# Kernel tuning notes

Measured on AMD Instinct MI355X. Metric: run time of the kernel, lower is better.

## Reference

```python
import jax, jax.numpy as jnp
import numpy as np

N_NODES = 100000
N_FEAT = 128
N_CLASSES = 40
N_EDGES = 1600000
K_HOPS = 2


def setup_inputs() -> dict:
    key = jax.random.key(0)
    k1, k2, k3 = jax.random.split(key, 3)
    x = jax.random.normal(k1, (N_NODES, N_FEAT), dtype=jnp.float32)
    edge_index = jax.random.randint(k2, (2, N_EDGES), 0, N_NODES, dtype=jnp.int32)
    W = jax.random.normal(k3, (N_FEAT, N_CLASSES), dtype=jnp.float32) * 0.05
    b = jnp.zeros((N_CLASSES,), dtype=jnp.float32)
    return {"x": x, "W": W, "b": b, "edge_index": edge_index, "K": K_HOPS}


def reference(x, W, b, edge_index, K):
    N = x.shape[0]
    src, dst = edge_index[0], edge_index[1]
    # Add self-loops (GCN normalization, as in PyG gcn_norm)
    loop = jnp.arange(N, dtype=src.dtype)
    src = jnp.concatenate([src, loop])
    dst = jnp.concatenate([dst, loop])
    # Symmetric normalization: deg^{-1/2} A_hat deg^{-1/2}
    deg = jnp.zeros((N,), dtype=x.dtype).at[dst].add(jnp.ones_like(dst, dtype=x.dtype))
    deg_inv_sqrt = jnp.where(deg > 0, jax.lax.rsqrt(jnp.maximum(deg, 1.0)), 0.0)
    norm = deg_inv_sqrt[src] * deg_inv_sqrt[dst]  # [E+N]
    for _ in range(K):
        msgs = norm[:, None] * x[src]  # gather [E+N, F]
        x = jax.ops.segment_sum(msgs, dst, num_segments=N)
    logits = x @ W + b  # [N, C]
    return jax.nn.log_softmax(logits, axis=1)
```

## Files before the change

kernel.cpp:

```cpp
#include <hip/hip_runtime.h>
#include <math.h>


#define FDIM 128
#define CDIM 40
#define C4   10
#define BKT_SHIFT 8
#define NB   512
#define NBLK 512
#define NPB  51

__device__ __forceinline__ unsigned int bf16rn(float f) {
    unsigned int u = __float_as_uint(f);
    return (u + 0x7fffu + ((u >> 16) & 1u)) >> 16;
}
__device__ __forceinline__ unsigned int pack2(float lo, float hi) {
    unsigned int a = bf16rn(lo);
    unsigned int b = __float_as_uint(hi);
    b = (b + 0x7fffu + ((b >> 16) & 1u)) & 0xffff0000u;
    return a | b;
}
__device__ __forceinline__ void addu4(uint4 u, float* a) {
    a[0] += __uint_as_float(u.x << 16);
    a[1] += __uint_as_float(u.x & 0xffff0000u);
    a[2] += __uint_as_float(u.y << 16);
    a[3] += __uint_as_float(u.y & 0xffff0000u);
    a[4] += __uint_as_float(u.z << 16);
    a[5] += __uint_as_float(u.z & 0xffff0000u);
    a[6] += __uint_as_float(u.w << 16);
    a[7] += __uint_as_float(u.w & 0xffff0000u);
}

__global__ void hist_k(const int* __restrict__ dst, int* __restrict__ G,
                       int E, int EB) {
    __shared__ int h[NB];
    int t = threadIdx.x;
    for (int i = t; i < NB; i += 256) h[i] = 0;
    __syncthreads();
    int s = blockIdx.x * EB;
    int e = min(s + EB, E);
    for (int i = s + t; i < e; i += 256)
        atomicAdd(&h[dst[i] >> BKT_SHIFT], 1);
    __syncthreads();
    for (int i = t; i < NB; i += 256) G[blockIdx.x * NB + i] = h[i];
}

__global__ void colscan_k(int* __restrict__ G, int* __restrict__ T) {
    __shared__ int lds[256];
    int j = blockIdx.x;
    int t = threadIdx.x;
    int v0 = G[(2 * t) * NB + j];
    int v1 = G[(2 * t + 1) * NB + j];
    int s = v0 + v1;
    lds[t] = s;
    __syncthreads();
    for (int off = 1; off < 256; off <<= 1) {
        int a = (t >= off) ? lds[t - off] : 0;
        __syncthreads();
        lds[t] += a;
        __syncthreads();
    }
    int excl = lds[t] - s;
    G[(2 * t) * NB + j] = excl;
    G[(2 * t + 1) * NB + j] = excl + v0;
    if (t == 255) T[j] = lds[255];
}

__global__ void bscan_k(const int* __restrict__ T, int* __restrict__ bs) {
    __shared__ int lds[256];
    int t = threadIdx.x;
    int v0 = T[2 * t];
    int v1 = T[2 * t + 1];
    int s = v0 + v1;
    lds[t] = s;
    __syncthreads();
    for (int off = 1; off < 256; off <<= 1) {
        int a = (t >= off) ? lds[t - off] : 0;
        __syncthreads();
        lds[t] += a;
        __syncthreads();
    }
    int excl = lds[t] - s;
    bs[2 * t] = excl;
    bs[2 * t + 1] = excl + v0;
    if (t == 255) bs[NB] = lds[255];
}

__global__ void part_k(const int* __restrict__ src, const int* __restrict__ dst,
                       const int* __restrict__ G, const int* __restrict__ bs,
                       unsigned int* __restrict__ tmp, int E, int EB) {
    __shared__ int offs[NB];
    __shared__ int cur[NB];
    int t = threadIdx.x;
    for (int i = t; i < NB; i += 256) {
        offs[i] = bs[i] + G[blockIdx.x * NB + i];
        cur[i] = 0;
    }
    __syncthreads();
    int s = blockIdx.x * EB;
    int e = min(s + EB, E);
    for (int i = s + t; i < e; i += 256) {
        int d = dst[i];
        int j = d >> BKT_SHIFT;
        int r = atomicAdd(&cur[j], 1);
        tmp[offs[j] + r] = (unsigned int)src[i] | ((unsigned int)(d & 255) << 24);
    }
}

__global__ void csr_k(const unsigned int* __restrict__ tmp, const int* __restrict__ bs,
                      int* __restrict__ rowptr, float* __restrict__ dinv,
                      float* __restrict__ dsq, int* __restrict__ col, int N, int E) {
    __shared__ int cnt[256];
    __shared__ int ptr[256];
    int j = blockIdx.x;
    int t = threadIdx.x;
    int base = j << BKT_SHIFT;
    int s = bs[j];
    int e = bs[j + 1];
    cnt[t] = 0;
    __syncthreads();
    for (int i = s + t; i < e; i += 256)
        atomicAdd(&cnt[tmp[i] >> 24], 1);
    __syncthreads();
    int v = cnt[t];
    ptr[t] = v;
    __syncthreads();
    for (int off = 1; off < 256; off <<= 1) {
        int a = (t >= off) ? ptr[t - off] : 0;
        __syncthreads();
        ptr[t] += a;
        __syncthreads();
    }
    int excl = ptr[t] - v;
    int node = base + t;
    if (node < N) {
        rowptr[node] = s + excl;
        float d = (float)(v + 1);
        dinv[node] = rsqrtf(d);
        dsq[node] = sqrtf(d);
    }
    if (j == 0 && t == 0) rowptr[N] = E;
    cnt[t] = excl;
    __syncthreads();
    for (int i = s + t; i < e; i += 256) {
        unsigned int p = tmp[i];
        int loc = p >> 24;
        int r = atomicAdd(&cnt[loc], 1);
        col[s + r] = (int)(p & 0xFFFFFF);
    }
}

__global__ __launch_bounds__(256) void gemm_k(const float* __restrict__ x,
                                              const float* __restrict__ W,
                                              const float* __restrict__ dinv,
                                              uint4* __restrict__ Zbf, int n) {
    int node = blockIdx.x * 256 + threadIdx.x;
    if (node >= n) return;
    float acc[CDIM];
    #pragma unroll
    for (int c = 0; c < CDIM; ++c) acc[c] = 0.f;
    const float4* xr = (const float4*)(x + (size_t)node * FDIM);
    for (int ch = 0; ch < 8; ++ch) {
        float4 xv0 = xr[ch * 4 + 0];
        float4 xv1 = xr[ch * 4 + 1];
        float4 xv2 = xr[ch * 4 + 2];
        float4 xv3 = xr[ch * 4 + 3];
        const float* wb = W + ch * 16 * CDIM;
        const float xs[16] = {xv0.x, xv0.y, xv0.z, xv0.w,
                              xv1.x, xv1.y, xv1.z, xv1.w,
                              xv2.x, xv2.y, xv2.z, xv2.w,
                              xv3.x, xv3.y, xv3.z, xv3.w};
        #pragma unroll
        for (int f = 0; f < 16; ++f) {
            float s = xs[f];
            const float* wr = wb + f * CDIM;
            #pragma unroll
            for (int c = 0; c < CDIM; ++c)
                acc[c] += s * wr[c];
        }
    }
    float di = dinv[node];
    uint4* zp = Zbf + (size_t)node * 5;
    #pragma unroll
    for (int g = 0; g < 5; ++g) {
        uint4 o;
        o.x = pack2(acc[g * 8 + 0] * di, acc[g * 8 + 1] * di);
        o.y = pack2(acc[g * 8 + 2] * di, acc[g * 8 + 3] * di);
        o.z = pack2(acc[g * 8 + 4] * di, acc[g * 8 + 5] * di);
        o.w = pack2(acc[g * 8 + 6] * di, acc[g * 8 + 7] * di);
        zp[g] = o;
    }
}

template <bool FINAL>
__global__ __launch_bounds__(256) void prop_k(const int* __restrict__ rowptr,
                                              const int* __restrict__ col,
                                              const float* __restrict__ dinv,
                                              const float* __restrict__ dsq,
                                              const float* __restrict__ bias,
                                              const uint4* __restrict__ Zin,
                                              uint4* __restrict__ Zout_bf,
                                              float* __restrict__ out_f32, int n) {
    __shared__ float bsm[CDIM];
    __shared__ float red[256];
    int t = threadIdx.x;
    if (FINAL && t < CDIM) bsm[t] = bias[t];
    int g = t / 5;
    int c8 = t - g * 5;
    int node = blockIdx.x * NPB + g;
    bool active = (g < NPB) && (node < n);
    float acc[8];
    #pragma unroll
    for (int c = 0; c < 8; ++c) acc[c] = 0.f;
    float w = 0.f;
    if (active) {
        float di = dinv[node];
        w = di * di;
        addu4(Zin[(size_t)node * 5 + c8], acc);
        int e = rowptr[node];
        int end = rowptr[node + 1];
        for (; e + 3 < end; e += 4) {
            int s0 = col[e], s1 = col[e + 1], s2 = col[e + 2], s3 = col[e + 3];
            uint4 a0 = Zin[(size_t)s0 * 5 + c8];
            uint4 a1 = Zin[(size_t)s1 * 5 + c8];
            uint4 a2 = Zin[(size_t)s2 * 5 + c8];
            uint4 a3 = Zin[(size_t)s3 * 5 + c8];
            addu4(a0, acc); addu4(a1, acc); addu4(a2, acc); addu4(a3, acc);
        }
        for (; e < end; ++e)
            addu4(Zin[(size_t)col[e] * 5 + c8], acc);
    }

    if (!FINAL) {
        if (active) {
            uint4 o;
            o.x = pack2(acc[0] * w, acc[1] * w);
            o.y = pack2(acc[2] * w, acc[3] * w);
            o.z = pack2(acc[4] * w, acc[5] * w);
            o.w = pack2(acc[6] * w, acc[7] * w);
            Zout_bf[(size_t)node * 5 + c8] = o;
        }
        return;
    }

    __syncthreads();
    float v[8];
    float m8 = -INFINITY;
    if (active) {
        float ws_ = w * dsq[node];
        #pragma unroll
        for (int j = 0; j < 8; ++j) {
            v[j] = acc[j] * ws_ + bsm[c8 * 8 + j];
            m8 = fmaxf(m8, v[j]);
        }
    }
    red[t] = m8;
    __syncthreads();
    float m = m8;
    if (active) {
        int rb = g * 5;
        m = fmaxf(fmaxf(fmaxf(red[rb], red[rb + 1]), fmaxf(red[rb + 2], red[rb + 3])),
                  red[rb + 4]);
    }
    float s8 = 0.f;
    if (active) {
        #pragma unroll
        for (int j = 0; j < 8; ++j) s8 += expf(v[j] - m);
    }
    __syncthreads();
    red[t] = s8;
    __syncthreads();
    if (active) {
        int rb = g * 5;
        float s = (red[rb] + red[rb + 1]) + (red[rb + 2] + red[rb + 3]) + red[rb + 4];
        float ls = m + logf(s);
        float* p = out_f32 + (size_t)node * CDIM + c8 * 8;
        *(float4*)p = make_float4(v[0] - ls, v[1] - ls, v[2] - ls, v[3] - ls);
        *(float4*)(p + 4) = make_float4(v[4] - ls, v[5] - ls, v[6] - ls, v[7] - ls);
    }
}

extern "C" void kernel_launch(void* const* d_in, const int* in_sizes, int n_in,
                              void* d_out, int out_size, void* d_ws, size_t ws_size,
                              hipStream_t stream) {
    const float* x = (const float*)d_in[0];
    const float* W = (const float*)d_in[1];
    const float* b = (const float*)d_in[2];
    const int* ei = (const int*)d_in[3];

    int C = in_sizes[2];
    int F = in_sizes[1] / C;
    int N = in_sizes[0] / F;
    int E = in_sizes[3] / 2;
    const int* src = ei;
    const int* dst = ei + E;

    char* ws = (char*)d_ws;
    size_t goff = 0;
    int* G = (int*)(ws + goff);                       goff += (size_t)NBLK * NB * 4;
    int* T = (int*)(ws + goff);                       goff += (size_t)NB * 4;
    int* bs = (int*)(ws + goff);                      goff += (size_t)(NB + 1) * 4 + 12;
    goff = (goff + 15) & ~(size_t)15;
    unsigned int* tmp = (unsigned int*)(ws + goff);   goff += (size_t)E * 4;
    size_t z0bytes = (size_t)N * 80;
    size_t unionEnd = (z0bytes > goff) ? z0bytes : goff;
    unionEnd = (unionEnd + 15) & ~(size_t)15;
    uint4* Z0bf = (uint4*)ws;
    size_t off = unionEnd;
    int* rowptr = (int*)(ws + off); off += ((size_t)(N + 1) * 4 + 15) & ~(size_t)15;
    float* dinv = (float*)(ws + off); off += ((size_t)N * 4 + 15) & ~(size_t)15;
    float* dsq = (float*)(ws + off); off += ((size_t)N * 4 + 15) & ~(size_t)15;
    int* col = (int*)(ws + off); off += ((size_t)E * 4 + 15) & ~(size_t)15;
    uint4* Zb = (uint4*)(ws + off); off += (z0bytes + 15) & ~(size_t)15;

    int EB = (E + NBLK - 1) / NBLK;
    int NBr = (N + 255) >> BKT_SHIFT;

    hist_k<<<NBLK, 256, 0, stream>>>(dst, G, E, EB);
    colscan_k<<<NB, 256, 0, stream>>>(G, T);
    bscan_k<<<1, 256, 0, stream>>>(T, bs);
    part_k<<<NBLK, 256, 0, stream>>>(src, dst, G, bs, tmp, E, EB);
    csr_k<<<NBr, 256, 0, stream>>>(tmp, bs, rowptr, dinv, dsq, col, N, E);

    gemm_k<<<(N + 255) / 256, 256, 0, stream>>>(x, W, dinv, Z0bf, N);

    int pgrid = (N + NPB - 1) / NPB;
    prop_k<false><<<pgrid, 256, 0, stream>>>(rowptr, col, dinv, dsq, b,
                                             Z0bf, Zb, nullptr, N);
    prop_k<true><<<pgrid, 256, 0, stream>>>(rowptr, col, dinv, dsq, b,
                                            Zb, nullptr, (float*)d_out, N);
}
```

Measured before the change: 248.4 us.

## Restructure dense projection to stage node tile in LDS and split classes across wavefronts

The projection kernel no longer has each thread compute all 40 outputs for one node from a privately loaded row. It now stages a 64-node tile of x transposed into shared memory, and five wavefronts each compute an 8-class slice with wave-uniform W loads. The aim is to cut per-thread register pressure (40 accumulators plus unrolled weights) and raise occupancy. The cost is a shared-memory transpose with strided writes, which may cause bank conflicts, plus a block-wide barrier.

```diff
diff --git a/kernel.cpp b/kernel.cpp
--- a/kernel.cpp
+++ b/kernel.cpp
@@ -150,45 +150,50 @@
     }
 }
 
-__global__ __launch_bounds__(256) void gemm_k(const float* __restrict__ x,
+__global__ __launch_bounds__(320) void gemm_k(const float* __restrict__ x,
                                               const float* __restrict__ W,
                                               const float* __restrict__ dinv,
                                               uint4* __restrict__ Zbf, int n) {
-    int node = blockIdx.x * 256 + threadIdx.x;
-    if (node >= n) return;
-    float acc[CDIM];
+    __shared__ float xT[FDIM][64];
+    int t = threadIdx.x;
+    int base = blockIdx.x * 64;
+    for (int i = t; i < 2048; i += 320) {
+        int nl = i & 63;
+        int f4 = i >> 6;
+        int node = base + nl;
+        float4 xv = make_float4(0.f, 0.f, 0.f, 0.f);
+        if (node < n) xv = *(const float4*)(x + (size_t)node * FDIM + f4 * 4);
+        xT[f4 * 4 + 0][nl] = xv.x;
+        xT[f4 * 4 + 1][nl] = xv.y;
+        xT[f4 * 4 + 2][nl] = xv.z;
+        xT[f4 * 4 + 3][nl] = xv.w;
+    }
+    int cg = __builtin_amdgcn_readfirstlane(t >> 6);
+    int ng = t & 63;
+    float acc[8];
     #pragma unroll
-    for (int c = 0; c < CDIM; ++c) acc[c] = 0.f;
-    const float4* xr = (const float4*)(x + (size_t)node * FDIM);
-    for (int ch = 0; ch < 8; ++ch) {
-        float4 xv0 = xr[ch * 4 + 0];
-        float4 xv1 = xr[ch * 4 + 1];
-        float4 xv2 = xr[ch * 4 + 2];
-        float4 xv3 = xr[ch * 4 + 3];
-        const float* wb = W + ch * 16 * CDIM;
-        const float xs[16] = {xv0.x, xv0.y, xv0.z, xv0.w,
-                              xv1.x, xv1.y, xv1.z, xv1.w,
-                              xv2.x, xv2.y, xv2.z, xv2.w,
-                              xv3.x, xv3.y, xv3.z, xv3.w};
-        #pragma unroll
-        for (int f = 0; f < 16; ++f) {
-            float s = xs[f];
-            const float* wr = wb + f * CDIM;
-            #pragma unroll
-            for (int c = 0; c < CDIM; ++c)
-                acc[c] += s * wr[c];
-        }
-    }
-    float di = dinv[node];
-    uint4* zp = Zbf + (size_t)node * 5;
-    #pragma unroll
-    for (int g = 0; g < 5; ++g) {
+    for (int c = 0; c < 8; ++c) acc[c] = 0.f;
+    __syncthreads();
+    const float* wbase = W + cg * 8;
+    #pragma unroll 4
+    for (int f = 0; f < FDIM; ++f) {
+        float xv = xT[f][ng];
+        float4 w0 = *(const float4*)(wbase + f * CDIM);
+        float4 w1 = *(const float4*)(wbase + f * CDIM + 4);
+        acc[0] += xv * w0.x; acc[1] += xv * w0.y;
+        acc[2] += xv * w0.z; acc[3] += xv * w0.w;
+        acc[4] += xv * w1.x; acc[5] += xv * w1.y;
+        acc[6] += xv * w1.z; acc[7] += xv * w1.w;
+    }
+    int node = base + ng;
+    if (node < n) {
+        float di = dinv[node];
         uint4 o;
-        o.x = pack2(acc[g * 8 + 0] * di, acc[g * 8 + 1] * di);
-        o.y = pack2(acc[g * 8 + 2] * di, acc[g * 8 + 3] * di);
-        o.z = pack2(acc[g * 8 + 4] * di, acc[g * 8 + 5] * di);
-        o.w = pack2(acc[g * 8 + 6] * di, acc[g * 8 + 7] * di);
-        zp[g] = o;
+        o.x = pack2(acc[0] * di, acc[1] * di);
+        o.y = pack2(acc[2] * di, acc[3] * di);
+        o.z = pack2(acc[4] * di, acc[5] * di);
+        o.w = pack2(acc[6] * di, acc[7] * di);
+        Zbf[(size_t)node * 5 + cg] = o;
     }
 }
 
@@ -322,7 +327,7 @@
     part_k<<<NBLK, 256, 0, stream>>>(src, dst, G, bs, tmp, E, EB);
     csr_k<<<NBr, 256, 0, stream>>>(tmp, bs, rowptr, dinv, dsq, col, N, E);
 
-    gemm_k<<<(N + 255) / 256, 256, 0, stream>>>(x, W, dinv, Z0bf, N);
+    gemm_k<<<(N + 63) / 64, 320, 0, stream>>>(x, W, dinv, Z0bf, N);
 
     int pgrid = (N + NPB - 1) / NPB;
     prop_k<false><<<pgrid, 256, 0, stream>>>(rowptr, col, dinv, dsq, b,
```

Result: faster. 233.6 us (-6.0%).

## Compute feature projection with split-bf16 MFMA instead of scalar FP32 FMAs

Applied to the files above, without the earlier changes.

Replaces the per-thread scalar FP32 GEMM (x @ W) with a wave-level MFMA 16x16x32 bf16 kernel. Both operands are split into bf16 hi and lo parts, and three products are summed to keep near-FP32 accuracy. A one-block prep kernel pre-swizzles W into the MFMA fragment layout. The epilogue stages results through shared memory so they can be scaled by dinv and packed to bf16. This targets the compute-bound scalar GEMM at the cost of an extra launch and some precision loss from the dropped lo*lo term.

```diff
diff --git a/kernel.cpp b/kernel.cpp
--- a/kernel.cpp
+++ b/kernel.cpp
@@ -9,6 +9,9 @@
 #define NB   512
 #define NBLK 512
 #define NPB  51
+
+typedef __attribute__((ext_vector_type(4))) float floatx4;
+typedef __attribute__((ext_vector_type(8))) short bshort8;
 
 __device__ __forceinline__ unsigned int bf16rn(float f) {
     unsigned int u = __float_as_uint(f);
@@ -150,45 +153,124 @@
     }
 }
 
+__global__ __launch_bounds__(256) void wprep_k(const float* __restrict__ W,
+                                               uint4* __restrict__ WF) {
+    int t = threadIdx.x;
+    for (int s = t; s < 768; s += 256) {
+        int l = s & 63;
+        int g = s >> 6;
+        int nt = g >> 2;
+        int ch = g & 3;
+        int c = nt * 16 + (l & 15);
+        int kb = ch * 32 + ((l >> 4) << 3);
+        unsigned int hw[4], lw[4];
+        #pragma unroll
+        for (int jw = 0; jw < 4; ++jw) {
+            unsigned int hs[2], ls[2];
+            #pragma unroll
+            for (int e = 0; e < 2; ++e) {
+                int j = jw * 2 + e;
+                float w = (c < CDIM) ? W[(kb + j) * CDIM + c] : 0.f;
+                unsigned int u = __float_as_uint(w);
+                float wh = __uint_as_float(u & 0xffff0000u);
+                float wr = w - wh;
+                hs[e] = u >> 16;
+                ls[e] = __float_as_uint(wr) >> 16;
+            }
+            hw[jw] = hs[0] | (hs[1] << 16);
+            lw[jw] = ls[0] | (ls[1] << 16);
+        }
+        WF[g * 64 + l] = make_uint4(hw[0], hw[1], hw[2], hw[3]);
+        WF[768 + g * 64 + l] = make_uint4(lw[0], lw[1], lw[2], lw[3]);
+    }
+}
+
+__device__ __forceinline__ void split8(const float* p, bshort8& hi, bshort8& lo) {
+    float4 a = *(const float4*)p;
+    float4 b = *(const float4*)(p + 4);
+    float f[8] = {a.x, a.y, a.z, a.w, b.x, b.y, b.z, b.w};
+    #pragma unroll
+    for (int j = 0; j < 8; ++j) {
+        unsigned int u = __float_as_uint(f[j]);
+        float r = f[j] - __uint_as_float(u & 0xffff0000u);
+        hi[j] = (short)(u >> 16);
+        lo[j] = (short)(__float_as_uint(r) >> 16);
+    }
+}
+
+#define EPS 52
+
 __global__ __launch_bounds__(256) void gemm_k(const float* __restrict__ x,
-                                              const float* __restrict__ W,
+                                              const uint4* __restrict__ WF,
                                               const float* __restrict__ dinv,
                                               uint4* __restrict__ Zbf, int n) {
-    int node = blockIdx.x * 256 + threadIdx.x;
-    if (node >= n) return;
-    float acc[CDIM];
+    __shared__ float ep[64 * EPS];
+    int t = threadIdx.x;
+    int wid = t >> 6;
+    int l = t & 63;
+    int lr = l & 15;
+    int lg = l >> 4;
+    int base64 = blockIdx.x * 64;
+    int mbase = base64 + wid * 16;
+    int node_a = mbase + lr;
+    bool arow_ok = node_a < n;
+    const bshort8* WFv = (const bshort8*)WF;
+
+    floatx4 acc0 = {0.f, 0.f, 0.f, 0.f};
+    floatx4 acc1 = {0.f, 0.f, 0.f, 0.f};
+    floatx4 acc2 = {0.f, 0.f, 0.f, 0.f};
+
     #pragma unroll
-    for (int c = 0; c < CDIM; ++c) acc[c] = 0.f;
-    const float4* xr = (const float4*)(x + (size_t)node * FDIM);
-    for (int ch = 0; ch < 8; ++ch) {
-        float4 xv0 = xr[ch * 4 + 0];
-        float4 xv1 = xr[ch * 4 + 1];
-        float4 xv2 = xr[ch * 4 + 2];
-        float4 xv3 = xr[ch * 4 + 3];
-        const float* wb = W + ch * 16 * CDIM;
-        const float xs[16] = {xv0.x, xv0.y, xv0.z, xv0.w,
-                              xv1.x, xv1.y, xv1.z, xv1.w,
-                              xv2.x, xv2.y, xv2.z, xv2.w,
-                              xv3.x, xv3.y, xv3.z, xv3.w};
-        #pragma unroll
-        for (int f = 0; f < 16; ++f) {
-            float s = xs[f];
-            const float* wr = wb + f * CDIM;
+    for (int ch = 0; ch < 4; ++ch) {
+        bshort8 ah, al;
+        if (arow_ok) {
+            split8(x + (size_t)node_a * FDIM + ch * 32 + lg * 8, ah, al);
+        } else {
             #pragma unroll
-            for (int c = 0; c < CDIM; ++c)
-                acc[c] += s * wr[c];
-        }
-    }
-    float di = dinv[node];
-    uint4* zp = Zbf + (size_t)node * 5;
+            for (int j = 0; j < 8; ++j) { ah[j] = 0; al[j] = 0; }
+        }
+        bshort8 bh0 = WFv[(0 * 4 + ch) * 64 + l];
+        bshort8 bl0 = WFv[768 + (0 * 4 + ch) * 64 + l];
+        bshort8 bh1 = WFv[(1 * 4 + ch) * 64 + l];
+        bshort8 bl1 = WFv[768 + (1 * 4 + ch) * 64 + l];
+        bshort8 bh2 = WFv[(2 * 4 + ch) * 64 + l];
+        bshort8 bl2 = WFv[768 + (2 * 4 + ch) * 64 + l];
+        acc0 = __builtin_amdgcn_mfma_f32_16x16x32_bf16(ah, bh0, acc0, 0, 0, 0);
+        acc0 = __builtin_amdgcn_mfma_f32_16x16x32_bf16(al, bh0, acc0, 0, 0, 0);
+        acc0 = __builtin_amdgcn_mfma_f32_16x16x32_bf16(ah, bl0, acc0, 0, 0, 0);
+        acc1 = __builtin_amdgcn_mfma_f32_16x16x32_bf16(ah, bh1, acc1, 0, 0, 0);
+        acc1 = __builtin_amdgcn_mfma_f32_16x16x32_bf16(al, bh1, acc1, 0, 0, 0);
+        acc1 = __builtin_amdgcn_mfma_f32_16x16x32_bf16(ah, bl1, acc1, 0, 0, 0);
+        acc2 = __builtin_amdgcn_mfma_f32_16x16x32_bf16(ah, bh2, acc2, 0, 0, 0);
+        acc2 = __builtin_amdgcn_mfma_f32_16x16x32_bf16(al, bh2, acc2, 0, 0, 0);
+        acc2 = __builtin_amdgcn_mfma_f32_16x16x32_bf16(ah, bl2, acc2, 0, 0, 0);
+    }
+
+    int nlb = wid * 16 + 4 * lg;
     #pragma unroll
-    for (int g = 0; g < 5; ++g) {
-        uint4 o;
-        o.x = pack2(acc[g * 8 + 0] * di, acc[g * 8 + 1] * di);
-        o.y = pack2(acc[g * 8 + 2] * di, acc[g * 8 + 3] * di);
-        o.z = pack2(acc[g * 8 + 4] * di, acc[g * 8 + 5] * di);
-        o.w = pack2(acc[g * 8 + 6] * di, acc[g * 8 + 7] * di);
-        zp[g] = o;
+    for (int r = 0; r < 4; ++r) {
+        int nd = mbase + 4 * lg + r;
+        float di = (nd < n) ? dinv[nd] : 0.f;
+        ep[(nlb + r) * EPS + 0 * 16 + lr] = acc0[r] * di;
+        ep[(nlb + r) * EPS + 1 * 16 + lr] = acc1[r] * di;
+        ep[(nlb + r) * EPS + 2 * 16 + lr] = acc2[r] * di;
+    }
+    __syncthreads();
+    for (int i = t; i < 320; i += 256) {
+        int nl2 = i / 5;
+        int cg = i - nl2 * 5;
+        int node = base64 + nl2;
+        if (node < n) {
+            const float* p = &ep[nl2 * EPS + cg * 8];
+            float4 v0 = *(const float4*)p;
+            float4 v1 = *(const float4*)(p + 4);
+            uint4 o;
+            o.x = pack2(v0.x, v0.y);
+            o.y = pack2(v0.z, v0.w);
+            o.z = pack2(v1.x, v1.y);
+            o.w = pack2(v1.z, v1.w);
+            Zbf[(size_t)node * 5 + cg] = o;
+        }
     }
 }
 
@@ -312,6 +394,7 @@
     float* dsq = (float*)(ws + off); off += ((size_t)N * 4 + 15) & ~(size_t)15;
     int* col = (int*)(ws + off); off += ((size_t)E * 4 + 15) & ~(size_t)15;
     uint4* Zb = (uint4*)(ws + off); off += (z0bytes + 15) & ~(size_t)15;
+    uint4* WF = (uint4*)(ws + off); off += (size_t)2 * 768 * 16;
 
     int EB = (E + NBLK - 1) / NBLK;
     int NBr = (N + 255) >> BKT_SHIFT;
@@ -322,7 +405,8 @@
     part_k<<<NBLK, 256, 0, stream>>>(src, dst, G, bs, tmp, E, EB);
     csr_k<<<NBr, 256, 0, stream>>>(tmp, bs, rowptr, dinv, dsq, col, N, E);
 
-    gemm_k<<<(N + 255) / 256, 256, 0, stream>>>(x, W, dinv, Z0bf, N);
+    wprep_k<<<1, 256, 0, stream>>>(W, WF);
+    gemm_k<<<(N + 63) / 64, 256, 0, stream>>>(x, WF, dinv, Z0bf, N);
 
     int pgrid = (N + NPB - 1) / NPB;
     prop_k<false><<<pgrid, 256, 0, stream>>>(rowptr, col, dinv, dsq, b,
```

Result: faster. 222.1 us (-10.6%).
